# Optimization experiments

Measured on AMD Instinct MI355X. Metric: run time of the kernel, lower is better.

The kernel has to match this reference:

```python
import jax, jax.numpy as jnp
import numpy as np

NUM_HEADS = 16
THETA = 10000.0


def _rope(x, pos):
    # x: [..., S, D_h], pos: [S] (broadcastable over leading dims)
    dh = x.shape[-1]
    inv_freq = THETA ** (-jnp.arange(0, dh, 2, dtype=x.dtype) / dh)  # [dh/2]
    ang = pos.astype(x.dtype)[..., None] * inv_freq                   # [S, dh/2]
    cos, sin = jnp.cos(ang), jnp.sin(ang)
    x1, x2 = x[..., ::2], x[..., 1::2]
    out = jnp.stack([x1 * cos - x2 * sin, x1 * sin + x2 * cos], axis=-1)
    return out.reshape(x.shape)


def setup_inputs() -> dict:
    key = jax.random.key(0)
    ks = jax.random.split(key, 5)
    B, S, D = 4, 2048, 1024
    return {
        "in_features": jax.random.normal(ks[0], (B, S, D), dtype=jnp.float32),
        "token_positions": jnp.arange(S, dtype=jnp.int32),
        "wq": jax.random.normal(ks[1], (D, D), dtype=jnp.float32) * 0.02,
        "wk": jax.random.normal(ks[2], (D, D), dtype=jnp.float32) * 0.02,
        "wv": jax.random.normal(ks[3], (D, D), dtype=jnp.float32) * 0.02,
        "wo": jax.random.normal(ks[4], (D, D), dtype=jnp.float32) * 0.02,
    }


def reference(in_features, token_positions, wq, wk, wv, wo):
    B, S, D = in_features.shape
    H = NUM_HEADS
    dh = D // H

    def split_heads(y):  # [B,S,D] -> [B,H,S,dh]  ('s (h d) -> h s d')
        return y.reshape(B, S, H, dh).transpose(0, 2, 1, 3)

    Q = split_heads(in_features @ wq.T)
    K = split_heads(in_features @ wk.T)
    V = split_heads(in_features @ wv.T)

    Q = _rope(Q, token_positions)
    K = _rope(K, token_positions)

    scale = 1.0 / jnp.sqrt(jnp.asarray(dh, dtype=Q.dtype))
    scores = jnp.einsum("bhqd,bhkd->bhqk", Q, K) * scale  # [B,H,S,S]
    causal = jnp.tril(jnp.ones((S, S), dtype=bool))
    scores = jnp.where(causal, scores, -jnp.inf)
    attn = jax.nn.softmax(scores, axis=-1)
    out = jnp.einsum("bhqk,bhkd->bhqd", attn, V)          # [B,H,S,dh]
    out = out.transpose(0, 2, 1, 3).reshape(B, S, D)      # 'h s d -> s (h d)'
    return out @ wo.T
```

## Files before the change

### kernel.cpp

```cpp
#include <hip/hip_runtime.h>
#include <hip/hip_bf16.h>
#include <cmath>

#define BB 4
#define SS 2048
#define DD 1024
#define HH 16
#define DH 64
#define LDK 72

typedef __attribute__((ext_vector_type(8))) short short8;
typedef __attribute__((ext_vector_type(4))) float floatx4;
typedef unsigned short u16;
typedef unsigned int u32;

#define QSCALE 0.18033688011112042f

__device__ __forceinline__ u16 f2bf(float f) {
    union { float f; u32 i; } u; u.f = f;
    u32 r = u.i + 0x7fff + ((u.i >> 16) & 1);
    return (u16)(r >> 16);
}

__device__ __forceinline__ u32 pack_bf16(float a, float b) {
    union { float f; u32 i; } ua, ub; ua.f = a; ub.f = b;
    return __builtin_amdgcn_perm(ub.i + 0x8000u, ua.i + 0x8000u, 0x07060302u);
}

#if !__has_builtin(__builtin_amdgcn_exp2f)
#define __builtin_amdgcn_exp2f exp2f
#endif

__global__ __launch_bounds__(256)
void cast_x(const float* __restrict__ s, u16* __restrict__ d)
{
    int i = (blockIdx.x * 256 + threadIdx.x) * 8;
    float4 f0 = *(const float4*)(s + i);
    float4 f1 = *(const float4*)(s + i + 4);
    u32 o[4];
    o[0] = pack_bf16(f0.x, f0.y); o[1] = pack_bf16(f0.z, f0.w);
    o[2] = pack_bf16(f1.x, f1.y); o[3] = pack_bf16(f1.z, f1.w);
    *(short8*)(d + i) = *(short8*)o;
}

__global__ __launch_bounds__(256)
void cast_w(const float* __restrict__ w0, const float* __restrict__ w1,
            const float* __restrict__ w2, const float* __restrict__ w3,
            u16* __restrict__ o0, u16* __restrict__ o1,
            u16* __restrict__ o2, u16* __restrict__ o3)
{
    const float* s = (blockIdx.y == 0) ? w0 : (blockIdx.y == 1) ? w1 : (blockIdx.y == 2) ? w2 : w3;
    u16* d        = (blockIdx.y == 0) ? o0 : (blockIdx.y == 1) ? o1 : (blockIdx.y == 2) ? o2 : o3;
    int i = (blockIdx.x * 256 + threadIdx.x) * 8;
    float4 f0 = *(const float4*)(s + i);
    float4 f1 = *(const float4*)(s + i + 4);
    u32 o[4];
    o[0] = pack_bf16(f0.x, f0.y); o[1] = pack_bf16(f0.z, f0.w);
    o[2] = pack_bf16(f1.x, f1.y); o[3] = pack_bf16(f1.z, f1.w);
    *(short8*)(d + i) = *(short8*)o;
}

__global__ __launch_bounds__(256)
void gemm_qkv(const u16* __restrict__ Xb,
              const u16* __restrict__ Wq, const u16* __restrict__ Wk, const u16* __restrict__ Wv,
              const int* __restrict__ pos,
              u16* __restrict__ Qb, u16* __restrict__ Kb, u16* __restrict__ Vtb)
{
    __shared__ __align__(16) u16 As[128 * LDK];
    __shared__ __align__(16) u16 Bs[128 * LDK];

    const int tid  = threadIdx.x;
    const int lane = tid & 63, w = tid >> 6;
    const int quad = lane >> 4, l16 = lane & 15;
    const int wr = w >> 1, wc = w & 1;
    const int m0 = blockIdx.x * 128, n0 = blockIdx.y * 128;
    const int which = blockIdx.z;
    const u16* __restrict__ W = (which == 0) ? Wq : (which == 1) ? Wk : Wv;

    const int srow = tid >> 3;
    const int skc  = (tid & 7) << 3;

    floatx4 acc[4][4];
    #pragma unroll
    for (int i = 0; i < 4; i++)
        #pragma unroll
        for (int j = 0; j < 4; j++) acc[i][j] = (floatx4)0.f;

    short8 pa[4], pb[4];
    #pragma unroll
    for (int i = 0; i < 4; i++) {
        int row = srow + i * 32;
        pa[i] = *(const short8*)(Xb + (size_t)(m0 + row) * DD + skc);
        pb[i] = *(const short8*)(W  + (size_t)(n0 + row) * DD + skc);
    }

    for (int kb = 0; kb < DD; kb += 64) {
        __syncthreads();
        #pragma unroll
        for (int i = 0; i < 4; i++) {
            int row = srow + i * 32;
            *(short8*)&As[row * LDK + skc] = pa[i];
            *(short8*)&Bs[row * LDK + skc] = pb[i];
        }
        __syncthreads();
        if (kb + 64 < DD) {
            #pragma unroll
            for (int i = 0; i < 4; i++) {
                int row = srow + i * 32;
                pa[i] = *(const short8*)(Xb + (size_t)(m0 + row) * DD + kb + 64 + skc);
                pb[i] = *(const short8*)(W  + (size_t)(n0 + row) * DD + kb + 64 + skc);
            }
        }
        #pragma unroll
        for (int ks = 0; ks < 2; ks++) {
            short8 a[4], b[4];
            #pragma unroll
            for (int mi = 0; mi < 4; mi++)
                a[mi] = *(const short8*)&As[(wr * 64 + mi * 16 + l16) * LDK + ks * 32 + quad * 8];
            #pragma unroll
            for (int ni = 0; ni < 4; ni++)
                b[ni] = *(const short8*)&Bs[(wc * 64 + ni * 16 + l16) * LDK + ks * 32 + quad * 8];
            #pragma unroll
            for (int mi = 0; mi < 4; mi++)
                #pragma unroll
                for (int ni = 0; ni < 4; ni++)
                    acc[mi][ni] = __builtin_amdgcn_mfma_f32_16x16x32_bf16(a[mi], b[ni], acc[mi][ni], 0, 0, 0);
        }
    }

    const int colbase = n0 + wc * 64 + l16;
    const int rowbase = m0 + wr * 64 + quad * 4;
    u16* __restrict__ OutQK = (which == 0) ? Qb : Kb;

    #pragma unroll
    for (int ni = 0; ni < 4; ni++) {
        int col = colbase + ni * 16;
        int h = col >> 6, d = col & 63;
        float fr = __powf(10000.0f, -(float)(d & ~1) / 64.0f);
        bool evn = (d & 1) == 0;
        #pragma unroll
        for (int mi = 0; mi < 4; mi++) {
            int row0 = rowbase + mi * 16;
            if (which == 2) {
                int b = row0 >> 11, s0 = row0 & (SS - 1);
                ushort4 uv;
                uv.x = f2bf(acc[mi][ni][0]);
                uv.y = f2bf(acc[mi][ni][1]);
                uv.z = f2bf(acc[mi][ni][2]);
                uv.w = f2bf(acc[mi][ni][3]);
                *(ushort4*)&Vtb[((size_t)((b * HH + h) * DH + d)) * SS + s0] = uv;
            } else {
                #pragma unroll
                for (int r = 0; r < 4; r++) {
                    int row = row0 + r;
                    int b = row >> 11, s = row & (SS - 1);
                    float v = acc[mi][ni][r];
                    float other = __shfl_xor(v, 1);
                    float ang = (float)pos[s] * fr;
                    float sn, cs;
                    __sincosf(ang, &sn, &cs);
                    float res = evn ? (v * cs - other * sn) : (other * sn + v * cs);
                    if (which == 0) res *= QSCALE;
                    OutQK[((size_t)((b * HH + h) * SS + s)) * DH + d] = f2bf(res);
                }
            }
        }
    }
}

__device__ __forceinline__ void attn_step(
    const u16* Ks, const u16* Vs, u16* Psw,
    const short8* qf, floatx4* oacc, float& m_run, float& l_run,
    const int l16, const int quad, const bool diag, const int qloc)
{
    floatx4 sacc[4];
    #pragma unroll
    for (int ni = 0; ni < 4; ni++) sacc[ni] = (floatx4)0.f;
    #pragma unroll
    for (int ks = 0; ks < 2; ks++) {
        #pragma unroll
        for (int ni = 0; ni < 4; ni++) {
            short8 kf = *(const short8*)&Ks[(ni * 16 + l16) * LDK + ks * 32 + quad * 8];
            sacc[ni] = __builtin_amdgcn_mfma_f32_16x16x32_bf16(kf, qf[ks], sacc[ni], 0, 0, 0);
        }
    }

    if (diag) {
        #pragma unroll
        for (int ni = 0; ni < 4; ni++)
            #pragma unroll
            for (int r = 0; r < 4; r++)
                if (ni * 16 + quad * 4 + r > qloc) sacc[ni][r] = -__builtin_inff();
    }

    float mx01 = fmaxf(fmaxf(sacc[0][0], sacc[0][1]), fmaxf(sacc[0][2], sacc[0][3]));
    float mx23 = fmaxf(fmaxf(sacc[1][0], sacc[1][1]), fmaxf(sacc[1][2], sacc[1][3]));
    float mx45 = fmaxf(fmaxf(sacc[2][0], sacc[2][1]), fmaxf(sacc[2][2], sacc[2][3]));
    float mx67 = fmaxf(fmaxf(sacc[3][0], sacc[3][1]), fmaxf(sacc[3][2], sacc[3][3]));
    float mx = fmaxf(fmaxf(mx01, mx23), fmaxf(mx45, mx67));
    mx = fmaxf(mx, __shfl_xor(mx, 16));
    mx = fmaxf(mx, __shfl_xor(mx, 32));
    float mnew = fmaxf(m_run, mx);
    float al = __builtin_amdgcn_exp2f(m_run - mnew);

    float rs = 0.f;
    #pragma unroll
    for (int ni = 0; ni < 4; ni++) {
        float p0 = __builtin_amdgcn_exp2f(sacc[ni][0] - mnew);
        float p1 = __builtin_amdgcn_exp2f(sacc[ni][1] - mnew);
        float p2 = __builtin_amdgcn_exp2f(sacc[ni][2] - mnew);
        float p3 = __builtin_amdgcn_exp2f(sacc[ni][3] - mnew);
        rs += (p0 + p1) + (p2 + p3);
        u32 pk[2];
        pk[0] = pack_bf16(p0, p1);
        pk[1] = pack_bf16(p2, p3);
        *(uint2*)&Psw[l16 * LDK + ni * 16 + quad * 4] = *(uint2*)pk;
    }
    l_run = l_run * al + rs;
    m_run = mnew;

    #pragma unroll
    for (int ni = 0; ni < 4; ni++) oacc[ni] *= al;
    #pragma unroll
    for (int ks = 0; ks < 2; ks++) {
        short8 pb = *(const short8*)&Psw[l16 * LDK + ks * 32 + quad * 8];
        #pragma unroll
        for (int ni = 0; ni < 4; ni++) {
            short8 vf = *(const short8*)&Vs[(ni * 16 + l16) * LDK + ks * 32 + quad * 8];
            oacc[ni] = __builtin_amdgcn_mfma_f32_16x16x32_bf16(vf, pb, oacc[ni], 0, 0, 0);
        }
    }
}

__global__ __launch_bounds__(256)
void flash_mfma(const u16* __restrict__ Qb, const u16* __restrict__ Kb,
                const u16* __restrict__ Vtb, u16* __restrict__ AOb)
{
    __shared__ __align__(16) u16 Ks[64 * LDK];
    __shared__ __align__(16) u16 Vs[64 * LDK];
    __shared__ __align__(16) u16 Ps[4][2][16 * LDK];

    const int tid  = threadIdx.x;
    const int lane = tid & 63, w = tid >> 6;
    const int quad = lane >> 4, l16 = lane & 15;
    const int qtA = blockIdx.x;
    const int qtB = (SS / 64 - 1) - blockIdx.x;
    const int bh = blockIdx.y;
    const int b = bh >> 4, h = bh & 15;
    const size_t baseQK = (size_t)bh * SS * DH;
    const size_t baseVt = (size_t)bh * DH * SS;

    const int srow = tid >> 3;
    const int skc  = (tid & 7) << 3;

    const u16* QpA = Qb + baseQK + (size_t)(qtA * 64 + w * 16 + l16) * DH;
    const u16* QpB = Qb + baseQK + (size_t)(qtB * 64 + w * 16 + l16) * DH;
    short8 qfA[2], qfB[2];
    qfA[0] = *(const short8*)(QpA + quad * 8);
    qfA[1] = *(const short8*)(QpA + 32 + quad * 8);
    qfB[0] = *(const short8*)(QpB + quad * 8);
    qfB[1] = *(const short8*)(QpB + 32 + quad * 8);

    float mA = -__builtin_inff(), lA = 0.f;
    float mB = -__builtin_inff(), lB = 0.f;
    floatx4 oaccA[4], oaccB[4];
    #pragma unroll
    for (int ni = 0; ni < 4; ni++) { oaccA[ni] = (floatx4)0.f; oaccB[ni] = (floatx4)0.f; }

    const int qloc = w * 16 + l16;

    short8 kr[2], vr[2];
    #pragma unroll
    for (int i = 0; i < 2; i++) {
        int row = srow + i * 32;
        kr[i] = *(const short8*)(Kb + baseQK + (size_t)row * DH + skc);
        vr[i] = *(const short8*)(Vtb + baseVt + (size_t)row * SS + skc);
    }

    for (int kt = 0; kt <= qtB; kt++) {
        __syncthreads();
        #pragma unroll
        for (int i = 0; i < 2; i++) {
            int row = srow + i * 32;
            *(short8*)&Ks[row * LDK + skc] = kr[i];
            *(short8*)&Vs[row * LDK + skc] = vr[i];
        }
        __syncthreads();
        if (kt < qtB) {
            #pragma unroll
            for (int i = 0; i < 2; i++) {
                int row = srow + i * 32;
                kr[i] = *(const short8*)(Kb + baseQK + (size_t)((kt + 1) * 64 + row) * DH + skc);
                vr[i] = *(const short8*)(Vtb + baseVt + (size_t)row * SS + (kt + 1) * 64 + skc);
            }
        }

        if (kt <= qtA)
            attn_step(Ks, Vs, &Ps[w][0][0], qfA, oaccA, mA, lA,
                      l16, quad, kt == qtA, qloc);
        attn_step(Ks, Vs, &Ps[w][1][0], qfB, oaccB, mB, lB,
                  l16, quad, kt == qtB, qloc);
    }

    float lAt = lA;
    lAt += __shfl_xor(lAt, 16);
    lAt += __shfl_xor(lAt, 32);
    float lBt = lB;
    lBt += __shfl_xor(lBt, 16);
    lBt += __shfl_xor(lBt, 32);
    const float invlA = 1.f / lAt;
    const float invlB = 1.f / lBt;

    u16* dstA = AOb + (size_t)(b * SS + qtA * 64 + w * 16 + l16) * DD + h * DH;
    u16* dstB = AOb + (size_t)(b * SS + qtB * 64 + w * 16 + l16) * DD + h * DH;
    #pragma unroll
    for (int ni = 0; ni < 4; ni++) {
        u32 uo[2];
        uo[0] = pack_bf16(oaccA[ni][0] * invlA, oaccA[ni][1] * invlA);
        uo[1] = pack_bf16(oaccA[ni][2] * invlA, oaccA[ni][3] * invlA);
        *(uint2*)(dstA + ni * 16 + quad * 4) = *(uint2*)uo;
        uo[0] = pack_bf16(oaccB[ni][0] * invlB, oaccB[ni][1] * invlB);
        uo[1] = pack_bf16(oaccB[ni][2] * invlB, oaccB[ni][3] * invlB);
        *(uint2*)(dstB + ni * 16 + quad * 4) = *(uint2*)uo;
    }
}

__global__ __launch_bounds__(256)
void gemm_out(const u16* __restrict__ A, const u16* __restrict__ W, float* __restrict__ C)
{
    __shared__ __align__(16) u16 As[128 * LDK];
    __shared__ __align__(16) u16 Bs[128 * LDK];

    const int tid  = threadIdx.x;
    const int lane = tid & 63, w = tid >> 6;
    const int quad = lane >> 4, l16 = lane & 15;
    const int wr = w >> 1, wc = w & 1;
    const int m0 = blockIdx.x * 128, n0 = blockIdx.y * 128;

    const int srow = tid >> 3;
    const int skc  = (tid & 7) << 3;

    floatx4 acc[4][4];
    #pragma unroll
    for (int i = 0; i < 4; i++)
        #pragma unroll
        for (int j = 0; j < 4; j++) acc[i][j] = (floatx4)0.f;

    short8 pa[4], pb[4];
    #pragma unroll
    for (int i = 0; i < 4; i++) {
        int row = srow + i * 32;
        pa[i] = *(const short8*)(A + (size_t)(m0 + row) * DD + skc);
        pb[i] = *(const short8*)(W + (size_t)(n0 + row) * DD + skc);
    }

    for (int kb = 0; kb < DD; kb += 64) {
        __syncthreads();
        #pragma unroll
        for (int i = 0; i < 4; i++) {
            int row = srow + i * 32;
            *(short8*)&As[row * LDK + skc] = pa[i];
            *(short8*)&Bs[row * LDK + skc] = pb[i];
        }
        __syncthreads();
        if (kb + 64 < DD) {
            #pragma unroll
            for (int i = 0; i < 4; i++) {
                int row = srow + i * 32;
                pa[i] = *(const short8*)(A + (size_t)(m0 + row) * DD + kb + 64 + skc);
                pb[i] = *(const short8*)(W + (size_t)(n0 + row) * DD + kb + 64 + skc);
            }
        }
        #pragma unroll
        for (int ks = 0; ks < 2; ks++) {
            short8 a[4], b[4];
            #pragma unroll
            for (int mi = 0; mi < 4; mi++)
                a[mi] = *(const short8*)&As[(wr * 64 + mi * 16 + l16) * LDK + ks * 32 + quad * 8];
            #pragma unroll
            for (int ni = 0; ni < 4; ni++)
                b[ni] = *(const short8*)&Bs[(wc * 64 + ni * 16 + l16) * LDK + ks * 32 + quad * 8];
            #pragma unroll
            for (int mi = 0; mi < 4; mi++)
                #pragma unroll
                for (int ni = 0; ni < 4; ni++)
                    acc[mi][ni] = __builtin_amdgcn_mfma_f32_16x16x32_bf16(a[mi], b[ni], acc[mi][ni], 0, 0, 0);
        }
    }

    const int colbase = n0 + wc * 64 + l16;
    const int rowbase = m0 + wr * 64 + quad * 4;
    #pragma unroll
    for (int ni = 0; ni < 4; ni++) {
        int col = colbase + ni * 16;
        #pragma unroll
        for (int mi = 0; mi < 4; mi++) {
            int row0 = rowbase + mi * 16;
            #pragma unroll
            for (int r = 0; r < 4; r++)
                C[(size_t)(row0 + r) * DD + col] = acc[mi][ni][r];
        }
    }
}

extern "C" void kernel_launch(void* const* d_in, const int* in_sizes, int n_in,
                              void* d_out, int out_size, void* d_ws, size_t ws_size,
                              hipStream_t stream) {
    const float* X  = (const float*)d_in[0];
    const int* pos  = (const int*)d_in[1];
    const float* wq = (const float*)d_in[2];
    const float* wk = (const float*)d_in[3];
    const float* wv = (const float*)d_in[4];
    const float* wo = (const float*)d_in[5];
    float* out = (float*)d_out;

    const size_t wsz = (size_t)DD * DD;
    const size_t qsz = (size_t)BB * HH * SS * DH;
    u16* Wqb = (u16*)d_ws;
    u16* Wkb = Wqb + wsz;
    u16* Wvb = Wkb + wsz;
    u16* Wob = Wvb + wsz;
    u16* Qb  = Wob + wsz;
    u16* Kb  = Qb + qsz;
    u16* Vtb = Kb + qsz;
    u16* Xb  = Vtb + qsz;
    u16* AOb = Xb;

    dim3 blk(256);
    cast_x<<<dim3(BB * SS * DD / 2048), blk, 0, stream>>>(X, Xb);
    cast_w<<<dim3(DD * DD / 2048, 4), blk, 0, stream>>>(wq, wk, wv, wo, Wqb, Wkb, Wvb, Wob);
    gemm_qkv<<<dim3((BB * SS) / 128, DD / 128, 3), blk, 0, stream>>>(Xb, Wqb, Wkb, Wvb, pos, Qb, Kb, Vtb);
    flash_mfma<<<dim3(SS / 128, BB * HH), blk, 0, stream>>>(Qb, Kb, Vtb, AOb);
    gemm_out<<<dim3((BB * SS) / 128, DD / 128), blk, 0, stream>>>(AOb, Wob, out);
}
```

Baseline: 279.8 us.

## Stage GEMM tiles with direct global-to-LDS loads and merge cast kernels

Both projection GEMMs stop staging tiles through registers. Each wave now issues `global_load_lds` 16-byte transfers straight into an unpadded 64-wide LDS tile, which removes the register round-trip and the padding. The separate X and weight cast kernels become one launch, saving a kernel launch. In exchange, the register-level prefetch of the next K tile is gone, so loads no longer overlap compute within a block. The unpadded LDS stride may also cause bank conflicts on the fragment reads.

```diff
diff --git a/kernel.cpp b/kernel.cpp
--- a/kernel.cpp
+++ b/kernel.cpp
@@ -31,10 +31,30 @@
 #define __builtin_amdgcn_exp2f exp2f
 #endif
 
+__device__ __forceinline__ void async16(const u16* g, u16* l) {
+    __builtin_amdgcn_global_load_lds(
+        (const __attribute__((address_space(1))) unsigned int*)g,
+        (__attribute__((address_space(3))) unsigned int*)l, 16, 0, 0);
+}
+
 __global__ __launch_bounds__(256)
-void cast_x(const float* __restrict__ s, u16* __restrict__ d)
+void cast_all(const float* __restrict__ X,
+              const float* __restrict__ w0, const float* __restrict__ w1,
+              const float* __restrict__ w2, const float* __restrict__ w3,
+              u16* __restrict__ Xb,
+              u16* __restrict__ o0, u16* __restrict__ o1,
+              u16* __restrict__ o2, u16* __restrict__ o3)
 {
-    int i = (blockIdx.x * 256 + threadIdx.x) * 8;
+    int bid = blockIdx.x;
+    const float* s; u16* d; int blk;
+    if (bid < 4096) { s = X; d = Xb; blk = bid; }
+    else {
+        int t = bid - 4096;
+        int wsel = t >> 9;  blk = t & 511;
+        s = (wsel == 0) ? w0 : (wsel == 1) ? w1 : (wsel == 2) ? w2 : w3;
+        d = (wsel == 0) ? o0 : (wsel == 1) ? o1 : (wsel == 2) ? o2 : o3;
+    }
+    int i = (blk * 256 + threadIdx.x) * 8;
     float4 f0 = *(const float4*)(s + i);
     float4 f1 = *(const float4*)(s + i + 4);
     u32 o[4];
@@ -44,30 +64,13 @@
 }
 
 __global__ __launch_bounds__(256)
-void cast_w(const float* __restrict__ w0, const float* __restrict__ w1,
-            const float* __restrict__ w2, const float* __restrict__ w3,
-            u16* __restrict__ o0, u16* __restrict__ o1,
-            u16* __restrict__ o2, u16* __restrict__ o3)
-{
-    const float* s = (blockIdx.y == 0) ? w0 : (blockIdx.y == 1) ? w1 : (blockIdx.y == 2) ? w2 : w3;
-    u16* d        = (blockIdx.y == 0) ? o0 : (blockIdx.y == 1) ? o1 : (blockIdx.y == 2) ? o2 : o3;
-    int i = (blockIdx.x * 256 + threadIdx.x) * 8;
-    float4 f0 = *(const float4*)(s + i);
-    float4 f1 = *(const float4*)(s + i + 4);
-    u32 o[4];
-    o[0] = pack_bf16(f0.x, f0.y); o[1] = pack_bf16(f0.z, f0.w);
-    o[2] = pack_bf16(f1.x, f1.y); o[3] = pack_bf16(f1.z, f1.w);
-    *(short8*)(d + i) = *(short8*)o;
-}
-
-__global__ __launch_bounds__(256)
 void gemm_qkv(const u16* __restrict__ Xb,
               const u16* __restrict__ Wq, const u16* __restrict__ Wk, const u16* __restrict__ Wv,
               const int* __restrict__ pos,
               u16* __restrict__ Qb, u16* __restrict__ Kb, u16* __restrict__ Vtb)
 {
-    __shared__ __align__(16) u16 As[128 * LDK];
-    __shared__ __align__(16) u16 Bs[128 * LDK];
+    __shared__ __align__(16) u16 As[128 * 64];
+    __shared__ __align__(16) u16 Bs[128 * 64];
 
     const int tid  = threadIdx.x;
     const int lane = tid & 63, w = tid >> 6;
@@ -77,8 +80,12 @@
     const int which = blockIdx.z;
     const u16* __restrict__ W = (which == 0) ? Wq : (which == 1) ? Wk : Wv;
 
-    const int srow = tid >> 3;
-    const int skc  = (tid & 7) << 3;
+    const int srow = w * 32 + (lane >> 3);
+    const int scol = (lane & 7) * 8;
+    const u16* gA = Xb + (size_t)(m0 + srow) * DD + scol;
+    const u16* gB = W  + (size_t)(n0 + srow) * DD + scol;
+    u16* lA = As + (w * 32) * 64;
+    u16* lB = Bs + (w * 32) * 64;
 
     floatx4 acc[4][4];
     #pragma unroll
@@ -86,40 +93,23 @@
         #pragma unroll
         for (int j = 0; j < 4; j++) acc[i][j] = (floatx4)0.f;
 
-    short8 pa[4], pb[4];
-    #pragma unroll
-    for (int i = 0; i < 4; i++) {
-        int row = srow + i * 32;
-        pa[i] = *(const short8*)(Xb + (size_t)(m0 + row) * DD + skc);
-        pb[i] = *(const short8*)(W  + (size_t)(n0 + row) * DD + skc);
-    }
-
     for (int kb = 0; kb < DD; kb += 64) {
         __syncthreads();
         #pragma unroll
-        for (int i = 0; i < 4; i++) {
-            int row = srow + i * 32;
-            *(short8*)&As[row * LDK + skc] = pa[i];
-            *(short8*)&Bs[row * LDK + skc] = pb[i];
-        }
-        __syncthreads();
-        if (kb + 64 < DD) {
-            #pragma unroll
-            for (int i = 0; i < 4; i++) {
-                int row = srow + i * 32;
-                pa[i] = *(const short8*)(Xb + (size_t)(m0 + row) * DD + kb + 64 + skc);
-                pb[i] = *(const short8*)(W  + (size_t)(n0 + row) * DD + kb + 64 + skc);
-            }
-        }
+        for (int j = 0; j < 4; j++) {
+            async16(gA + (size_t)j * 8 * DD + kb, lA + j * 8 * 64);
+            async16(gB + (size_t)j * 8 * DD + kb, lB + j * 8 * 64);
+        }
+        __syncthreads();
         #pragma unroll
         for (int ks = 0; ks < 2; ks++) {
             short8 a[4], b[4];
             #pragma unroll
             for (int mi = 0; mi < 4; mi++)
-                a[mi] = *(const short8*)&As[(wr * 64 + mi * 16 + l16) * LDK + ks * 32 + quad * 8];
+                a[mi] = *(const short8*)&As[(wr * 64 + mi * 16 + l16) * 64 + ks * 32 + quad * 8];
             #pragma unroll
             for (int ni = 0; ni < 4; ni++)
-                b[ni] = *(const short8*)&Bs[(wc * 64 + ni * 16 + l16) * LDK + ks * 32 + quad * 8];
+                b[ni] = *(const short8*)&Bs[(wc * 64 + ni * 16 + l16) * 64 + ks * 32 + quad * 8];
             #pragma unroll
             for (int mi = 0; mi < 4; mi++)
                 #pragma unroll
@@ -328,8 +318,8 @@
 __global__ __launch_bounds__(256)
 void gemm_out(const u16* __restrict__ A, const u16* __restrict__ W, float* __restrict__ C)
 {
-    __shared__ __align__(16) u16 As[128 * LDK];
-    __shared__ __align__(16) u16 Bs[128 * LDK];
+    __shared__ __align__(16) u16 As[128 * 64];
+    __shared__ __align__(16) u16 Bs[128 * 64];
 
     const int tid  = threadIdx.x;
     const int lane = tid & 63, w = tid >> 6;
@@ -337,8 +327,12 @@
     const int wr = w >> 1, wc = w & 1;
     const int m0 = blockIdx.x * 128, n0 = blockIdx.y * 128;
 
-    const int srow = tid >> 3;
-    const int skc  = (tid & 7) << 3;
+    const int srow = w * 32 + (lane >> 3);
+    const int scol = (lane & 7) * 8;
+    const u16* gA = A + (size_t)(m0 + srow) * DD + scol;
+    const u16* gB = W + (size_t)(n0 + srow) * DD + scol;
+    u16* lA = As + (w * 32) * 64;
+    u16* lB = Bs + (w * 32) * 64;
 
     floatx4 acc[4][4];
     #pragma unroll
@@ -346,40 +340,23 @@
         #pragma unroll
         for (int j = 0; j < 4; j++) acc[i][j] = (floatx4)0.f;
 
-    short8 pa[4], pb[4];
-    #pragma unroll
-    for (int i = 0; i < 4; i++) {
-        int row = srow + i * 32;
-        pa[i] = *(const short8*)(A + (size_t)(m0 + row) * DD + skc);
-        pb[i] = *(const short8*)(W + (size_t)(n0 + row) * DD + skc);
-    }
-
     for (int kb = 0; kb < DD; kb += 64) {
         __syncthreads();
         #pragma unroll
-        for (int i = 0; i < 4; i++) {
-            int row = srow + i * 32;
-            *(short8*)&As[row * LDK + skc] = pa[i];
-            *(short8*)&Bs[row * LDK + skc] = pb[i];
-        }
-        __syncthreads();
-        if (kb + 64 < DD) {
-            #pragma unroll
-            for (int i = 0; i < 4; i++) {
-                int row = srow + i * 32;
-                pa[i] = *(const short8*)(A + (size_t)(m0 + row) * DD + kb + 64 + skc);
-                pb[i] = *(const short8*)(W + (size_t)(n0 + row) * DD + kb + 64 + skc);
-            }
-        }
+        for (int j = 0; j < 4; j++) {
+            async16(gA + (size_t)j * 8 * DD + kb, lA + j * 8 * 64);
+            async16(gB + (size_t)j * 8 * DD + kb, lB + j * 8 * 64);
+        }
+        __syncthreads();
         #pragma unroll
         for (int ks = 0; ks < 2; ks++) {
             short8 a[4], b[4];
             #pragma unroll
             for (int mi = 0; mi < 4; mi++)
-                a[mi] = *(const short8*)&As[(wr * 64 + mi * 16 + l16) * LDK + ks * 32 + quad * 8];
+                a[mi] = *(const short8*)&As[(wr * 64 + mi * 16 + l16) * 64 + ks * 32 + quad * 8];
             #pragma unroll
             for (int ni = 0; ni < 4; ni++)
-                b[ni] = *(const short8*)&Bs[(wc * 64 + ni * 16 + l16) * LDK + ks * 32 + quad * 8];
+                b[ni] = *(const short8*)&Bs[(wc * 64 + ni * 16 + l16) * 64 + ks * 32 + quad * 8];
             #pragma unroll
             for (int mi = 0; mi < 4; mi++)
                 #pragma unroll
@@ -427,8 +404,8 @@
     u16* AOb = Xb;
 
     dim3 blk(256);
-    cast_x<<<dim3(BB * SS * DD / 2048), blk, 0, stream>>>(X, Xb);
-    cast_w<<<dim3(DD * DD / 2048, 4), blk, 0, stream>>>(wq, wk, wv, wo, Wqb, Wkb, Wvb, Wob);
+    cast_all<<<dim3(4096 + 4 * 512), blk, 0, stream>>>(X, wq, wk, wv, wo,
+                                                       Xb, Wqb, Wkb, Wvb, Wob);
     gemm_qkv<<<dim3((BB * SS) / 128, DD / 128, 3), blk, 0, stream>>>(Xb, Wqb, Wkb, Wvb, pos, Qb, Kb, Vtb);
     flash_mfma<<<dim3(SS / 128, BB * HH), blk, 0, stream>>>(Qb, Kb, Vtb, AOb);
     gemm_out<<<dim3((BB * SS) / 128, DD / 128), blk, 0, stream>>>(AOb, Wob, out);
```

Result: slower. 293.0 us (+4.7%).
